# Kernel optimization log

Hardware: AMD Instinct MI355X
Metric: run time of the kernel (lower is better)

## Reference

```python
import jax, jax.numpy as jnp
import numpy as np

N_NODES = 70839  # num_user + num_item from config
N_EDGES = 2_000_000
EMB_DIM = 64
EPS = 1e-12  # torch F.normalize default eps


def setup_inputs() -> dict:
    key = jax.random.key(0)
    k1, k2, k3, k4 = jax.random.split(key, 4)
    ego_embedding = jax.random.normal(k1, (N_NODES, EMB_DIM), dtype=jnp.float32)
    edge_weight = jax.random.uniform(k2, (N_EDGES,), dtype=jnp.float32)
    edge_src = jax.random.randint(k3, (N_EDGES,), 0, N_NODES, dtype=jnp.int32)
    edge_dst = jax.random.randint(k4, (N_EDGES,), 0, N_NODES, dtype=jnp.int32)
    return {
        "ego_embedding": ego_embedding,
        "edge_weight": edge_weight,
        "edge_src": edge_src,
        "edge_dst": edge_dst,
    }


def reference(ego_embedding, edge_weight, edge_src, edge_dst):
    # message: m_e = h[src_e] * w_e   (u_mul_e)
    m = ego_embedding[edge_src] * edge_weight[:, None]          # [E, D]
    # reduce: h_v = sum_{e: dst_e = v} m_e   (fn.sum)
    h = jax.ops.segment_sum(m, edge_dst, num_segments=N_NODES)  # [N, D]
    # F.normalize(h, dim=1, p=2): x / max(||x||_2, eps)
    norm = jnp.linalg.norm(h, axis=1, keepdims=True)
    return h / jnp.maximum(norm, EPS)
```

## Files before the change

### kernel.cpp

```cpp
#include <hip/hip_runtime.h>
#include <hip/hip_fp16.h>

#define EMB_D 64
#define SB 1024
#define SPAN 128
#define SPAN_SH 7
#define MAXG 1024
#define NCHUNK2 512
#define CHMAX 4096
#define TILE 4096
#define CAST_BLOCKS 256
#define HIST_BLOCKS 128


__device__ __forceinline__ float h15_to_float(unsigned int bits) {
    return __half2float(__ushort_as_half((unsigned short)bits));
}

__device__ __forceinline__ uint4 rowld(const char* base, unsigned int pk,
                                       unsigned int qlo) {
    return *reinterpret_cast<const uint4*>(base + ((pk >> 15) * 128u + qlo));
}

__device__ __forceinline__ void fma8(float4& a, float4& b, uint4 r, float wt) {
    float2 x01 = __half22float2(*reinterpret_cast<__half2*>(&r.x));
    float2 x23 = __half22float2(*reinterpret_cast<__half2*>(&r.y));
    float2 x45 = __half22float2(*reinterpret_cast<__half2*>(&r.z));
    float2 x67 = __half22float2(*reinterpret_cast<__half2*>(&r.w));
    a.x = fmaf(x01.x, wt, a.x); a.y = fmaf(x01.y, wt, a.y);
    a.z = fmaf(x23.x, wt, a.z); a.w = fmaf(x23.y, wt, a.w);
    b.x = fmaf(x45.x, wt, b.x); b.y = fmaf(x45.y, wt, b.y);
    b.z = fmaf(x67.x, wt, b.z); b.w = fmaf(x67.y, wt, b.w);
}

__global__ void f1_cast_hist(const float4* __restrict__ embin,
                             uint2* __restrict__ emb16, int n4,
                             const int* __restrict__ dst,
                             int* __restrict__ hist,
                             int E, int G, int hchunk) {
    if (blockIdx.x < CAST_BLOCKS) {
        int i = blockIdx.x * blockDim.x + threadIdx.x;
        int st = CAST_BLOCKS * blockDim.x;
        for (; i < n4; i += st) {
            float4 v = embin[i];
            __half2 h0 = __float22half2_rn(make_float2(v.x, v.y));
            __half2 h1 = __float22half2_rn(make_float2(v.z, v.w));
            emb16[i] = make_uint2(*reinterpret_cast<unsigned int*>(&h0),
                                  *reinterpret_cast<unsigned int*>(&h1));
        }
    } else {
        __shared__ int bins[MAXG];
        int hb = blockIdx.x - CAST_BLOCKS;
        for (int g = threadIdx.x; g < G; g += blockDim.x) bins[g] = 0;
        __syncthreads();
        int beg = hb * hchunk;
        int end = min(beg + hchunk, E);
        for (int i = beg + threadIdx.x; i < end; i += blockDim.x)
            atomicAdd(&bins[dst[i] >> SPAN_SH], 1);
        __syncthreads();
        for (int g = threadIdx.x; g < G; g += blockDim.x)
            if (bins[g]) atomicAdd(&hist[g], bins[g]);
    }
}

__global__ void f2_scan_small(const int* __restrict__ hist,
                              int* __restrict__ offsets,
                              int* __restrict__ cursors, int G) {
    __shared__ int wsum[16];
    __shared__ int wpre[16];
    const int tid = threadIdx.x, lane = tid & 63, wid = tid >> 6;
    int v = (tid < G) ? hist[tid] : 0;
    int x = v;
    #pragma unroll
    for (int off = 1; off < 64; off <<= 1) {
        int t = __shfl_up(x, off, 64);
        if (lane >= off) x += t;
    }
    if (lane == 63) wsum[wid] = x;
    __syncthreads();
    if (wid == 0) {
        int s = (lane < 16) ? wsum[lane] : 0;
        #pragma unroll
        for (int off = 1; off < 16; off <<= 1) {
            int t = __shfl_up(s, off, 64);
            if (lane >= off) s += t;
        }
        if (lane < 16) wpre[lane] = s;
    }
    __syncthreads();
    int excl = ((wid > 0) ? wpre[wid - 1] : 0) + (x - v);
    if (tid < G) { offsets[tid] = excl; cursors[tid] = excl; }
    if (tid == 0) offsets[G] = wpre[15];
}

__global__ __launch_bounds__(512) void partition_atomic(
        const int* __restrict__ src,
        const int* __restrict__ dst,
        const float* __restrict__ w,
        int* __restrict__ cursors,
        uint2* __restrict__ stream8,
        int E, int G, int chunk) {
    __shared__ uint2 recs[CHMAX];
    __shared__ int cur[MAXG];
    __shared__ int delta[MAXG];
    __shared__ int wtot[8];

    const int tid = threadIdx.x, lane = tid & 63, wv = tid >> 6;
    const int b = blockIdx.x;
    const int c = (b & 7) * (NCHUNK2 >> 3) + (b >> 3);
    const int beg = c * chunk;
    const int end = min(beg + chunk, E);
    const int n = end - beg;

    for (int g = tid; g < G; g += 512) cur[g] = 0;
    __syncthreads();
    for (int i = beg + tid; i < end; i += 512)
        atomicAdd(&cur[dst[i] >> SPAN_SH], 1);
    __syncthreads();

    const int K = (G + 511) >> 9;
    int vals[2];
    int acc = 0;
    #pragma unroll
    for (int k = 0; k < 2; ++k) {
        int g = tid * K + k;
        int cc = (k < K && g < G) ? cur[g] : 0;
        vals[k] = cc;
        acc += cc;
    }
    int x = acc;
    #pragma unroll
    for (int off = 1; off < 64; off <<= 1) {
        int t = __shfl_up(x, off, 64);
        if (lane >= off) x += t;
    }
    if (lane == 63) wtot[wv] = x;
    __syncthreads();
    int woff = 0;
    #pragma unroll
    for (int k2 = 0; k2 < 8; ++k2)
        woff += (k2 < wv) ? wtot[k2] : 0;
    int run = woff + x - acc;
    #pragma unroll
    for (int k = 0; k < 2; ++k) {
        int g = tid * K + k;
        if (k < K && g < G) {
            int cc = vals[k];
            cur[g] = run;
            if (cc > 0)
                delta[g] = atomicAdd(&cursors[g], cc) - run;
            run += cc;
        }
    }
    __syncthreads();

    for (int i = beg + tid; i < end; i += 512) {
        int d = dst[i];
        unsigned int wb = __half_as_ushort(__float2half_rn(w[i]));
        unsigned int pk = ((unsigned int)src[i] << 15) | (wb & 0x7FFFu);
        int g = d >> SPAN_SH;
        int j = atomicAdd(&cur[g], 1);
        recs[j] = make_uint2(pk, (unsigned int)(d & (SPAN - 1)) |
                                 ((unsigned int)g << SPAN_SH));
    }
    __syncthreads();

    for (int j = tid; j < n; j += 512) {
        uint2 r = recs[j];
        int g = (int)(r.y >> SPAN_SH);
        stream8[delta[g] + j] = make_uint2(r.x, r.y & (SPAN - 1u));
    }
}

__global__ __launch_bounds__(512) void gather_fused(
        const char* __restrict__ emb16b,
        const uint2* __restrict__ stream8,
        const int* __restrict__ offsets,
        float* __restrict__ out, int N) {
    __shared__ uint2 lrec[TILE];
    __shared__ unsigned int srt[TILE];
    __shared__ int hcnt[SPAN];
    __shared__ int nstart[SPAN];
    __shared__ int cur[SPAN];
    __shared__ int wtot[2];

    const int g = blockIdx.x;
    const int tid = threadIdx.x;
    const int lane = tid & 63, wv = tid >> 6;
    const int base = offsets[g];
    const int endE = offsets[g + 1];
    const int crew = tid >> 4;
    const int ql = tid & 15;
    const int sub = ql >> 3;
    const int sl = ql & 7;
    const unsigned qlo = (unsigned)(sl << 4);

    float4 accA[4], accB[4];
    #pragma unroll
    for (int ni = 0; ni < 4; ++ni) {
        accA[ni] = make_float4(0.f, 0.f, 0.f, 0.f);
        accB[ni] = make_float4(0.f, 0.f, 0.f, 0.f);
    }

    for (int tb = base; tb < endE; tb += TILE) {
        const int n = min(TILE, endE - tb);
        if (tid < SPAN) hcnt[tid] = 0;
        __syncthreads();
        for (int j = tid; j < n; j += 512) {
            uint2 r = stream8[tb + j];
            lrec[j] = r;
            atomicAdd(&hcnt[r.y], 1);
        }
        __syncthreads();
        int v = (tid < SPAN) ? hcnt[tid] : 0;
        int x = v;
        #pragma unroll
        for (int off = 1; off < 64; off <<= 1) {
            int t = __shfl_up(x, off, 64);
            if (lane >= off) x += t;
        }
        if (wv < 2 && lane == 63) wtot[wv] = x;
        __syncthreads();
        if (tid < SPAN) {
            int excl = x - v + ((wv == 1) ? wtot[0] : 0);
            nstart[tid] = excl;
            cur[tid] = excl;
        }
        __syncthreads();
        for (int j = tid; j < n; j += 512) {
            uint2 r = lrec[j];
            int slot = atomicAdd(&cur[r.y], 1);
            srt[slot] = r.x;
        }
        __syncthreads();
        #pragma unroll
        for (int ni = 0; ni < 4; ++ni) {
            int nd = crew + (ni << 5);
            int s = nstart[nd];
            int e = cur[nd];
            float4 aA = accA[ni];
            float4 aB = accB[ni];
            int k0 = s + sub;
            unsigned int pk0 = (k0 < e) ? srt[k0] : 0u;
            uint4 r0 = rowld(emb16b, pk0, qlo);
            for (int k = k0; k < e; k += 2) {
                int k1 = k + 2;
                unsigned int pk1 = (k1 < e) ? srt[k1] : 0u;
                uint4 r1 = rowld(emb16b, pk1, qlo);
                fma8(aA, aB, r0, h15_to_float(pk0 & 0x7FFFu));
                pk0 = pk1; r0 = r1;
            }
            accA[ni] = aA;
            accB[ni] = aB;
        }
        __syncthreads();
    }

    #pragma unroll
    for (int ni = 0; ni < 4; ++ni) {
        accA[ni].x += __shfl_xor(accA[ni].x, 8, 64);
        accA[ni].y += __shfl_xor(accA[ni].y, 8, 64);
        accA[ni].z += __shfl_xor(accA[ni].z, 8, 64);
        accA[ni].w += __shfl_xor(accA[ni].w, 8, 64);
        accB[ni].x += __shfl_xor(accB[ni].x, 8, 64);
        accB[ni].y += __shfl_xor(accB[ni].y, 8, 64);
        accB[ni].z += __shfl_xor(accB[ni].z, 8, 64);
        accB[ni].w += __shfl_xor(accB[ni].w, 8, 64);
        int node = g * SPAN + crew + (ni << 5);
        float4 aA = accA[ni];
        float4 aB = accB[ni];
        float ss = aA.x * aA.x + aA.y * aA.y + aA.z * aA.z + aA.w * aA.w
                 + aB.x * aB.x + aB.y * aB.y + aB.z * aB.z + aB.w * aB.w;
        ss += __shfl_xor(ss, 1, 64);
        ss += __shfl_xor(ss, 2, 64);
        ss += __shfl_xor(ss, 4, 64);
        float scale = 1.0f / fmaxf(sqrtf(ss), 1e-12f);
        if (node < N) {
            float4 a = sub ? aB : aA;
            float4 o = make_float4(a.x * scale, a.y * scale,
                                   a.z * scale, a.w * scale);
            *reinterpret_cast<float4*>(out + (size_t)node * EMB_D
                                       + (sl << 3) + (sub << 2)) = o;
        }
    }
}

__global__ void lightgcn_scatter(const float* __restrict__ emb,
                                 const float* __restrict__ w,
                                 const int* __restrict__ src,
                                 const int* __restrict__ dst,
                                 float* __restrict__ h, int E) {
    long long t = (long long)blockIdx.x * blockDim.x + threadIdx.x;
    int e = (int)(t >> 4);
    int d = (int)(t & 15) << 2;
    if (e >= E) return;
    int s = src[e]; int v = dst[e]; float wt = w[e];
    const float4 m = *reinterpret_cast<const float4*>(emb + (size_t)s * EMB_D + d);
    float* o = h + (size_t)v * EMB_D + d;
    unsafeAtomicAdd(o + 0, m.x * wt);
    unsafeAtomicAdd(o + 1, m.y * wt);
    unsafeAtomicAdd(o + 2, m.z * wt);
    unsafeAtomicAdd(o + 3, m.w * wt);
}

__global__ void lightgcn_normalize(float* __restrict__ h, int N) {
    int row = blockIdx.x * (blockDim.x >> 6) + (threadIdx.x >> 6);
    int lane = threadIdx.x & 63;
    if (row >= N) return;
    float x = h[(size_t)row * EMB_D + lane];
    float ss = x * x;
    #pragma unroll
    for (int off = 32; off > 0; off >>= 1)
        ss += __shfl_xor(ss, off, 64);
    h[(size_t)row * EMB_D + lane] = x / fmaxf(sqrtf(ss), 1e-12f);
}

extern "C" void kernel_launch(void* const* d_in, const int* in_sizes, int n_in,
                              void* d_out, int out_size, void* d_ws, size_t ws_size,
                              hipStream_t stream) {
    const float* emb = (const float*)d_in[0];
    const float* w   = (const float*)d_in[1];
    const int*   src = (const int*)d_in[2];
    const int*   dst = (const int*)d_in[3];
    float* out = (float*)d_out;

    const int N = in_sizes[0] / EMB_D;
    const int E = in_sizes[1];
    const int block = 256;
    const int G = (N + SPAN - 1) / SPAN;
    const int chunk = (E + NCHUNK2 - 1) / NCHUNK2;
    const int hchunk = (E + HIST_BLOCKS - 1) / HIST_BLOCKS;

    size_t ints = 3 * (size_t)G + 1;
    size_t strOff = (ints * sizeof(int) + 15) & ~(size_t)15;
    size_t embOff = (strOff + (size_t)E * sizeof(uint2) + 15) & ~(size_t)15;
    size_t needed = embOff + (size_t)N * EMB_D * sizeof(__half);

    if (ws_size >= needed && G <= MAXG && chunk <= CHMAX &&
        E < (1 << 28) && N < (1 << 17)) {
        int* hist    = (int*)d_ws;
        int* offsets = hist + G;
        int* cursors = offsets + G + 1;
        uint2* stream8 = (uint2*)((char*)d_ws + strOff);
        uint2* emb16 = (uint2*)((char*)d_ws + embOff);

        int n4 = N * (EMB_D / 4);

        hipMemsetAsync(hist, 0, (size_t)G * sizeof(int), stream);

        f1_cast_hist<<<CAST_BLOCKS + HIST_BLOCKS, block, 0, stream>>>(
            (const float4*)emb, emb16, n4, dst, hist, E, G, hchunk);

        f2_scan_small<<<1, SB, 0, stream>>>(hist, offsets, cursors, G);

        partition_atomic<<<NCHUNK2, 512, 0, stream>>>(src, dst, w, cursors,
                                                      stream8, E, G, chunk);

        gather_fused<<<G, 512, 0, stream>>>((const char*)emb16, stream8,
                                            offsets, out, N);
    } else {
        hipMemsetAsync(d_out, 0, (size_t)out_size * sizeof(float), stream);
        long long total = (long long)E * 16;
        int grid = (int)((total + block - 1) / block);
        lightgcn_scatter<<<grid, block, 0, stream>>>(emb, w, src, dst, out, E);
        int gridN = (N + 3) / 4;
        lightgcn_normalize<<<gridN, 256, 0, stream>>>(out, N);
    }
}
```

Before: 182.5 us.

## Reuse per-chunk destination histograms in partition instead of recounting

The histogram pass now computes per-chunk bucket counts matching the partition chunks and stores them transposed in workspace. A new rowsum kernel reduces these into global bucket totals, replacing the global atomics and the memset. The partition kernel reads its per-chunk counts from this table instead of re-reading dst and recounting with shared atomics. The cost is an extra kernel launch, a larger workspace, and strided writes and reads of a G×512 count table.

```diff
diff --git a/kernel.cpp b/kernel.cpp
--- a/kernel.cpp
+++ b/kernel.cpp
@@ -2,7 +2,6 @@
 #include <hip/hip_fp16.h>
 
 #define EMB_D 64
-#define SB 1024
 #define SPAN 128
 #define SPAN_SH 7
 #define MAXG 1024
@@ -10,7 +9,6 @@
 #define CHMAX 4096
 #define TILE 4096
 #define CAST_BLOCKS 256
-#define HIST_BLOCKS 128
 
 
 __device__ __forceinline__ float h15_to_float(unsigned int bits) {
@@ -33,11 +31,11 @@
     b.z = fmaf(x67.x, wt, b.z); b.w = fmaf(x67.y, wt, b.w);
 }
 
-__global__ void f1_cast_hist(const float4* __restrict__ embin,
+__global__ void a1_cast_hist(const float4* __restrict__ embin,
                              uint2* __restrict__ emb16, int n4,
                              const int* __restrict__ dst,
-                             int* __restrict__ hist,
-                             int E, int G, int hchunk) {
+                             int* __restrict__ cntT,
+                             int E, int G, int chunk) {
     if (blockIdx.x < CAST_BLOCKS) {
         int i = blockIdx.x * blockDim.x + threadIdx.x;
         int st = CAST_BLOCKS * blockDim.x;
@@ -53,14 +51,29 @@
         int hb = blockIdx.x - CAST_BLOCKS;
         for (int g = threadIdx.x; g < G; g += blockDim.x) bins[g] = 0;
         __syncthreads();
-        int beg = hb * hchunk;
-        int end = min(beg + hchunk, E);
+        int beg = hb * chunk;
+        int end = min(beg + chunk, E);
         for (int i = beg + threadIdx.x; i < end; i += blockDim.x)
             atomicAdd(&bins[dst[i] >> SPAN_SH], 1);
         __syncthreads();
         for (int g = threadIdx.x; g < G; g += blockDim.x)
-            if (bins[g]) atomicAdd(&hist[g], bins[g]);
-    }
+            cntT[g * NCHUNK2 + hb] = bins[g];
+    }
+}
+
+__global__ void rowsum_kernel(const int* __restrict__ cntT,
+                              int* __restrict__ hist, int G) {
+    __shared__ int wsum[4];
+    const int g = blockIdx.x;
+    const int tid = threadIdx.x, lane = tid & 63, wid = tid >> 6;
+    int s = cntT[g * NCHUNK2 + tid] + cntT[g * NCHUNK2 + tid + 256];
+    #pragma unroll
+    for (int off = 32; off > 0; off >>= 1)
+        s += __shfl_xor(s, off, 64);
+    if (lane == 0) wsum[wid] = s;
+    __syncthreads();
+    if (tid == 0)
+        hist[g] = wsum[0] + wsum[1] + wsum[2] + wsum[3];
 }
 
 __global__ void f2_scan_small(const int* __restrict__ hist,
@@ -93,10 +106,11 @@
     if (tid == 0) offsets[G] = wpre[15];
 }
 
-__global__ __launch_bounds__(512) void partition_atomic(
+__global__ __launch_bounds__(512) void partition_res(
         const int* __restrict__ src,
         const int* __restrict__ dst,
         const float* __restrict__ w,
+        const int* __restrict__ cntT,
         int* __restrict__ cursors,
         uint2* __restrict__ stream8,
         int E, int G, int chunk) {
@@ -112,19 +126,13 @@
     const int end = min(beg + chunk, E);
     const int n = end - beg;
 
-    for (int g = tid; g < G; g += 512) cur[g] = 0;
-    __syncthreads();
-    for (int i = beg + tid; i < end; i += 512)
-        atomicAdd(&cur[dst[i] >> SPAN_SH], 1);
-    __syncthreads();
-
     const int K = (G + 511) >> 9;
     int vals[2];
     int acc = 0;
     #pragma unroll
     for (int k = 0; k < 2; ++k) {
         int g = tid * K + k;
-        int cc = (k < K && g < G) ? cur[g] : 0;
+        int cc = (k < K && g < G) ? cntT[g * NCHUNK2 + c] : 0;
         vals[k] = cc;
         acc += cc;
     }
@@ -329,16 +337,16 @@
     const int block = 256;
     const int G = (N + SPAN - 1) / SPAN;
     const int chunk = (E + NCHUNK2 - 1) / NCHUNK2;
-    const int hchunk = (E + HIST_BLOCKS - 1) / HIST_BLOCKS;
-
-    size_t ints = 3 * (size_t)G + 1;
+
+    size_t ints = (size_t)G * NCHUNK2 + 3 * (size_t)G + 1;
     size_t strOff = (ints * sizeof(int) + 15) & ~(size_t)15;
     size_t embOff = (strOff + (size_t)E * sizeof(uint2) + 15) & ~(size_t)15;
     size_t needed = embOff + (size_t)N * EMB_D * sizeof(__half);
 
     if (ws_size >= needed && G <= MAXG && chunk <= CHMAX &&
         E < (1 << 28) && N < (1 << 17)) {
-        int* hist    = (int*)d_ws;
+        int* cntT    = (int*)d_ws;
+        int* hist    = cntT + (size_t)G * NCHUNK2;
         int* offsets = hist + G;
         int* cursors = offsets + G + 1;
         uint2* stream8 = (uint2*)((char*)d_ws + strOff);
@@ -346,15 +354,14 @@
 
         int n4 = N * (EMB_D / 4);
 
-        hipMemsetAsync(hist, 0, (size_t)G * sizeof(int), stream);
-
-        f1_cast_hist<<<CAST_BLOCKS + HIST_BLOCKS, block, 0, stream>>>(
-            (const float4*)emb, emb16, n4, dst, hist, E, G, hchunk);
-
-        f2_scan_small<<<1, SB, 0, stream>>>(hist, offsets, cursors, G);
-
-        partition_atomic<<<NCHUNK2, 512, 0, stream>>>(src, dst, w, cursors,
-                                                      stream8, E, G, chunk);
+        a1_cast_hist<<<CAST_BLOCKS + NCHUNK2, block, 0, stream>>>(
+            (const float4*)emb, emb16, n4, dst, cntT, E, G, chunk);
+
+        rowsum_kernel<<<G, 256, 0, stream>>>(cntT, hist, G);
+        f2_scan_small<<<1, 1024, 0, stream>>>(hist, offsets, cursors, G);
+
+        partition_res<<<NCHUNK2, 512, 0, stream>>>(src, dst, w, cntT, cursors,
+                                                   stream8, E, G, chunk);
 
         gather_fused<<<G, 512, 0, stream>>>((const char*)emb16, stream8,
                                             offsets, out, N);
```

Measured after the change: 176.5 us, median of 2. -3.3%, faster.
